# Kernel tuning notes

Hardware: AMD Instinct MI355X
Metric: run time of the kernel (lower is better)

## Reference

```python
import jax, jax.numpy as jnp
import numpy as np

NEG_INF = -1e30  # stands in for -inf; safe under fp16/bf16 softmax too


def setup_inputs() -> dict:
    key = jax.random.key(0)
    k1, k2, k3, k4 = jax.random.split(key, 4)
    B, M, N, V, A = 16, 512, 512, 1024, 1024
    q = jax.random.normal(k1, (B, M, V), dtype=jnp.float32)
    p = jax.random.normal(k2, (B, N, V), dtype=jnp.float32)
    q_mask = jnp.ones((B, M), dtype=jnp.int32)  # 1 = real token
    p_mask = jnp.ones((B, N), dtype=jnp.int32)
    # xavier_normal: std = sqrt(2/(fan_in+fan_out))
    std = np.sqrt(2.0 / (V + A)).astype(np.float32)
    W1 = jax.random.normal(k3, (A, V), dtype=jnp.float32) * std
    W2 = jax.random.normal(k4, (A, V), dtype=jnp.float32) * std
    return {"q": q, "p": p, "q_mask": q_mask, "p_mask": p_mask, "W1": W1, "W2": W2}


def reference(q, p, q_mask, p_mask, W1, W2):
    # Projections with ReLU (bias-free linears)
    s_q = jax.nn.relu(jnp.einsum('bmv,av->bma', q, W1))  # [B,M,A]
    s_p = jax.nn.relu(jnp.einsum('bnv,av->bna', p, W2))  # [B,N,A]
    # Shared score matrix s[b,m,n]
    s = jnp.einsum('bma,bna->bmn', s_q, s_p)
    # Direction 1: attend over p (mask pad columns of p), softmax over n
    s_to_p = jnp.where(p_mask[:, None, :] == 0, NEG_INF, s)
    weights_p = jax.nn.softmax(s_to_p, axis=2)            # [B,M,N]
    output_q = jnp.einsum('bmn,bnv->bmv', weights_p, p)   # [B,M,V]
    # Direction 2: transpose, attend over q (mask pad columns of q)
    s_to_q = jnp.where(q_mask[:, None, :] == 0, NEG_INF, jnp.swapaxes(s, 1, 2))
    weights_q = jax.nn.softmax(s_to_q, axis=2)            # [B,N,M]
    output_p = jnp.einsum('bnm,bmv->bnv', weights_q, q)   # [B,N,V]
    # Dropout is identity in eval mode (training=False)
    return (output_p, output_q)
```

## Files before the change

kernel.cpp:

```cpp
#include <hip/hip_runtime.h>


#define AS1 __attribute__((address_space(1)))
#define AS3 __attribute__((address_space(3)))

typedef _Float16 f16x8 __attribute__((ext_vector_type(8)));
typedef float f32x4 __attribute__((ext_vector_type(4)));

__device__ __forceinline__ long tswz(int r, int k, int ktiles) {
  return ((long)((r >> 7) * ktiles + (k >> 6 ? (k >> 5) : (k >> 5))) << 12)
       + ((long)(r & 127) << 5)
       + ((((k >> 3) & 3) ^ ((r >> 1) & 3)) << 3) + (k & 7);
}

__global__ __launch_bounds__(256) void prep_all(
    const float* __restrict__ q, const float* __restrict__ p,
    const float* __restrict__ W1, const float* __restrict__ W2,
    _Float16* __restrict__ xdst, _Float16* __restrict__ wdst)
{
  long g = (long)blockIdx.x * 256 + threadIdx.x;
  int rg = (int)(g >> 7);
  int c8 = ((int)g & 127) << 3;
  const float* srow;
  _Float16* dst;
  long off;
  if (rg < 8192) {
    srow = q + (long)rg * 1024 + c8; dst = xdst; off = tswz(rg, c8, 32);
  } else if (rg < 16384) {
    srow = p + (long)(rg - 8192) * 1024 + c8; dst = xdst; off = tswz(rg, c8, 32);
  } else {
    int r2 = rg - 16384;
    srow = (r2 < 1024 ? W1 + (long)r2 * 1024 : W2 + (long)(r2 - 1024) * 1024) + c8;
    dst = wdst; off = tswz(r2, c8, 32);
  }
  const float4* s4 = (const float4*)srow;
  float4 f0 = s4[0], f1 = s4[1];
  f16x8 hh;
  hh[0]=(_Float16)f0.x; hh[1]=(_Float16)f0.y; hh[2]=(_Float16)f0.z; hh[3]=(_Float16)f0.w;
  hh[4]=(_Float16)f1.x; hh[5]=(_Float16)f1.y; hh[6]=(_Float16)f1.z; hh[7]=(_Float16)f1.w;
  *(f16x8*)(dst + off) = hh;
}

__global__ __launch_bounds__(256) void prep_xT(
    const float* __restrict__ q, const float* __restrict__ p,
    _Float16* __restrict__ dstT)
{
  __shared__ float t[64][65];
  const int x = blockIdx.x, y = blockIdx.y, zz = blockIdx.z;
  const float* src = (zz < 16) ? (p + (long)zz * 524288)
                               : (q + (long)(zz - 16) * 524288);
  const int tid = threadIdx.x;
  for (int it = 0; it < 4; ++it) {
    int id = it * 256 + tid;
    int rr = id >> 4, cc = (id & 15) << 2;
    float4 f = *(const float4*)(src + (long)(y * 64 + rr) * 1024 + x * 64 + cc);
    t[rr][cc] = f.x; t[rr][cc + 1] = f.y; t[rr][cc + 2] = f.z; t[rr][cc + 3] = f.w;
  }
  __syncthreads();
  _Float16* db = dstT + (long)zz * 524288;
  for (int it = 0; it < 2; ++it) {
    int id = it * 256 + tid;
    int c = id >> 3, ch = id & 7;
    int v = x * 64 + c, mb = y * 64 + ch * 8;
    f16x8 hh;
#pragma unroll
    for (int i = 0; i < 8; ++i) hh[i] = (_Float16)t[ch * 8 + i][c];
    *(f16x8*)(db + tswz(v, mb, 16)) = hh;
  }
}

template<bool RELU, int OUTMODE>
__global__ __launch_bounds__(512, 2) void gemm256_dp(
    const _Float16* __restrict__ A, const _Float16* __restrict__ B,
    float* __restrict__ Cf, _Float16* __restrict__ Ch,
    const int ktiles, const int ldc,
    const long aBatchTiles, const long bBatchTiles, const long cBatchElems,
    const int cTilesRow, const long cOff0, const long cOff1, const int cSplit)
{
  __shared__ _Float16 sA[4][8192];
  __shared__ _Float16 sB[4][8192];

  const int gx = gridDim.x, gy = gridDim.y;
  long nwg = (long)gx * gy * gridDim.z;
  long bid = blockIdx.x + (long)gx * (blockIdx.y + (long)gy * blockIdx.z);
  long chunk = nwg >> 3;
  long o = (bid & 7) * chunk + (bid >> 3);
  const int bx = (int)(o % gx);
  const int by = (int)((o / gx) % gy);
  const int bz = (int)(o / ((long)gx * gy));

  const int tid = threadIdx.x;
  const int lane = tid & 63, w = tid >> 6;
  const int wm = w >> 2, wn = w & 3;
  const int lrow = lane & 15, kg = lane >> 4;
  const int swz = (lrow >> 1) & 3;

  const long aT0 = (long)bz * aBatchTiles + (long)(2 * by) * ktiles;
  const long bT0 = (long)bz * bBatchTiles + (long)(2 * bx) * ktiles;
  const int NKT = ktiles;

  auto stage = [&](int kt) {
    const int buf = kt & 3;
#pragma unroll
    for (int h = 0; h < 2; ++h) {
      __builtin_amdgcn_global_load_lds(
          (const AS1 void*)(A + ((aT0 + h * ktiles + kt) << 12) + w * 512 + lane * 8),
          (AS3 void*)(&sA[buf][h * 4096 + w * 512]), 16, 0, 0);
      __builtin_amdgcn_global_load_lds(
          (const AS1 void*)(B + ((bT0 + h * ktiles + kt) << 12) + w * 512 + lane * 8),
          (AS3 void*)(&sB[buf][h * 4096 + w * 512]), 16, 0, 0);
    }
  };

  const char* aF = (const char*)&sA[0][0] + wm * 8192 + lrow * 64 + ((kg ^ swz) << 4);
  const char* bF = (const char*)&sB[0][0] + (wn >> 1) * 8192
                 + ((wn & 1) * 64 + lrow) * 64 + ((kg ^ swz) << 4);

  f32x4 acc[8][4] = {};

  stage(0); stage(1); stage(2);

  for (int kt = 0; kt < NKT; ++kt) {
    if (kt < NKT - 2)       asm volatile("s_waitcnt vmcnt(8)" ::: "memory");
    else if (kt == NKT - 2) asm volatile("s_waitcnt vmcnt(4)" ::: "memory");
    else                    asm volatile("s_waitcnt vmcnt(0)" ::: "memory");
    __builtin_amdgcn_s_barrier();
    __builtin_amdgcn_sched_barrier(0);
    const int bo = (kt & 3) * 16384;
    f16x8 fa[8], fb[4];
#pragma unroll
    for (int i = 0; i < 8; ++i) fa[i] = *(const f16x8*)(aF + bo + i * 1024);
#pragma unroll
    for (int i = 0; i < 4; ++i) fb[i] = *(const f16x8*)(bF + bo + i * 1024);
    if (kt + 3 < NKT) stage(kt + 3);
    __builtin_amdgcn_s_setprio(1);
    if (OUTMODE == 1) {
#pragma unroll
      for (int aj = 0; aj < 8; ++aj)
#pragma unroll
        for (int bi = 0; bi < 4; ++bi)
          acc[aj][bi] = __builtin_amdgcn_mfma_f32_16x16x32_f16(fb[bi], fa[aj], acc[aj][bi], 0, 0, 0);
    } else {
#pragma unroll
      for (int mi = 0; mi < 8; ++mi)
#pragma unroll
        for (int ni = 0; ni < 4; ++ni)
          acc[mi][ni] = __builtin_amdgcn_mfma_f32_16x16x32_f16(fa[mi], fb[ni], acc[mi][ni], 0, 0, 0);
    }
    __builtin_amdgcn_s_setprio(0);
  }

  if (OUTMODE == 1) {
    long cbase = cSplit ? (bz < 16 ? cOff0 + (long)bz * cBatchElems
                                   : cOff1 + (long)(bz - 16) * cBatchElems)
                        : (long)bz * cBatchElems;
    float* Cb = Cf + cbase;
    const int m0 = by * 256 + wm * 128 + lrow;
    const int v0 = bx * 256 + wn * 64 + (kg << 2);
#pragma unroll
    for (int aj = 0; aj < 8; ++aj)
#pragma unroll
      for (int bi = 0; bi < 4; ++bi)
        *(f32x4*)(Cb + (long)(m0 + aj * 16) * ldc + v0 + bi * 16) = acc[aj][bi];
  } else {
    const int m0 = by * 256 + wm * 128 + (kg << 2);
    const int a0 = bx * 256 + wn * 64 + lrow;
#pragma unroll
    for (int mi = 0; mi < 8; ++mi)
#pragma unroll
      for (int ni = 0; ni < 4; ++ni)
#pragma unroll
        for (int r2 = 0; r2 < 4; ++r2) {
          int r = m0 + mi * 16 + r2, c = a0 + ni * 16;
          float x = acc[mi][ni][r2];
          if (RELU) x = fmaxf(x, 0.0f);
          Ch[(long)bz * cBatchElems + tswz(r, c, cTilesRow)] = (_Float16)x;
        }
  }
}

template<int NTERMS, bool RELU>
__global__ __launch_bounds__(256, 2) void gemm_dp(
    const _Float16* __restrict__ Ah, const _Float16* __restrict__ Al,
    const _Float16* __restrict__ B, float* __restrict__ Cf,
    const int ktiles, const int ldc,
    const long aBatchTiles, const long bBatchTiles, const long cBatchElems)
{
  __shared__ _Float16 sA[4][4096];
  __shared__ _Float16 sB[4][4096];

  const int gx = gridDim.x, gy = gridDim.y;
  long nwg = (long)gx * gy * gridDim.z;
  long bid = blockIdx.x + (long)gx * (blockIdx.y + (long)gy * blockIdx.z);
  long chunk = nwg >> 3;
  long o = (bid & 7) * chunk + (bid >> 3);
  const int bx = (int)(o % gx);
  const int by = (int)((o / gx) % gy);
  const int bz = (int)(o / ((long)gx * gy));

  const int tid = threadIdx.x;
  const int lane = tid & 63, w = tid >> 6;
  const int wa = w >> 1, wb = w & 1;
  const int lrow = lane & 15, kg = lane >> 4;
  const int swz = (lrow >> 1) & 3;

  const long aT0 = (long)bz * aBatchTiles + (long)by * ktiles;
  const long bT0 = (long)bz * bBatchTiles + (long)bx * ktiles;
  const int NKT = NTERMS * ktiles;

  auto stage = [&](int kt) {
    const int buf = kt & 3;
    int ktB = kt;
    const _Float16* As = Ah;
    if (NTERMS == 2 && kt >= ktiles) { As = Al; ktB = kt - ktiles; }
    const long ta = (aT0 + ktB) << 12;
    const long tb = (bT0 + ktB) << 12;
#pragma unroll
    for (int j = 0; j < 2; ++j) {
      __builtin_amdgcn_global_load_lds(
          (const AS1 void*)(As + ta + j * 2048 + w * 512 + lane * 8),
          (AS3 void*)(&sA[buf][j * 2048 + w * 512]), 16, 0, 0);
      __builtin_amdgcn_global_load_lds(
          (const AS1 void*)(B + tb + j * 2048 + w * 512 + lane * 8),
          (AS3 void*)(&sB[buf][j * 2048 + w * 512]), 16, 0, 0);
    }
  };

  const char* aF = (const char*)&sA[0][0] + (wa * 64 + lrow) * 64 + ((kg ^ swz) << 4);
  const char* bF = (const char*)&sB[0][0] + (wb * 64 + lrow) * 64 + ((kg ^ swz) << 4);

  f32x4 acc[4][4] = {};

  stage(0); stage(1); stage(2);

  for (int kt = 0; kt < NKT; ++kt) {
    if (kt < NKT - 2)       asm volatile("s_waitcnt vmcnt(8)" ::: "memory");
    else if (kt == NKT - 2) asm volatile("s_waitcnt vmcnt(4)" ::: "memory");
    else                    asm volatile("s_waitcnt vmcnt(0)" ::: "memory");
    __builtin_amdgcn_s_barrier();
    __builtin_amdgcn_sched_barrier(0);
    const int bo = (kt & 3) * 8192;
    f16x8 fa[4], fb[4];
#pragma unroll
    for (int i = 0; i < 4; ++i) fa[i] = *(const f16x8*)(aF + bo + i * 1024);
#pragma unroll
    for (int i = 0; i < 4; ++i) fb[i] = *(const f16x8*)(bF + bo + i * 1024);
    if (kt + 3 < NKT) stage(kt + 3);
    __builtin_amdgcn_s_setprio(1);
#pragma unroll
    for (int mi = 0; mi < 4; ++mi)
#pragma unroll
      for (int ni = 0; ni < 4; ++ni)
        acc[mi][ni] = __builtin_amdgcn_mfma_f32_16x16x32_f16(fa[mi], fb[ni], acc[mi][ni], 0, 0, 0);
    __builtin_amdgcn_s_setprio(0);
  }

  float* Cb = Cf + (long)bz * cBatchElems;
  const int r0 = by * 128 + wa * 64 + (kg << 2);
  const int c0 = bx * 128 + wb * 64 + lrow;
#pragma unroll
  for (int mi = 0; mi < 4; ++mi)
#pragma unroll
    for (int ni = 0; ni < 4; ++ni)
#pragma unroll
      for (int r2 = 0; r2 < 4; ++r2)
        Cb[(long)(r0 + mi * 16 + r2) * ldc + c0 + ni * 16] = acc[mi][ni][r2];
}

__global__ __launch_bounds__(256) void softmax_row(
    const float* __restrict__ S, const int* __restrict__ mask, _Float16* __restrict__ W)
{
  const int row = blockIdx.x, b = row >> 9, m = row & 511;
  const float* Sr = S + (long)row * 512;
  const int* mr = mask + (long)b * 512;
  const int tid = threadIdx.x;
  const int lane = tid & 63, wave = tid >> 6;
  __shared__ float red[4];

  float v0 = mr[tid] ? Sr[tid] : -1e30f;
  float v1 = mr[tid + 256] ? Sr[tid + 256] : -1e30f;
  float mx = fmaxf(v0, v1);
#pragma unroll
  for (int of = 32; of >= 1; of >>= 1) mx = fmaxf(mx, __shfl_xor(mx, of, 64));
  if (lane == 0) red[wave] = mx;
  __syncthreads();
  mx = fmaxf(fmaxf(red[0], red[1]), fmaxf(red[2], red[3]));
  __syncthreads();
  float e0 = __expf(v0 - mx), e1 = __expf(v1 - mx);
  float sm = e0 + e1;
#pragma unroll
  for (int of = 32; of >= 1; of >>= 1) sm += __shfl_xor(sm, of, 64);
  if (lane == 0) red[wave] = sm;
  __syncthreads();
  float inv = 1.0f / (red[0] + red[1] + red[2] + red[3]);

  _Float16* Wb = W + (long)b * 262144;
  Wb[tswz(m, tid, 16)] = (_Float16)(e0 * inv);
  Wb[tswz(m, tid + 256, 16)] = (_Float16)(e1 * inv);
}

__global__ __launch_bounds__(256) void softmax_col(
    const float* __restrict__ S, const int* __restrict__ mask, _Float16* __restrict__ W)
{
  __shared__ float ldsT[32][513];
  const int n0 = blockIdx.x * 32, b = blockIdx.y;
  const float* Sb = S + (long)b * 262144;
  const int* mr = mask + (long)b * 512;
  const int tid = threadIdx.x;
  const int lane = tid & 63, w = tid >> 6;

  for (int it = 0; it < 64; ++it) {
    int m = it * 8 + (tid >> 5);
    int c = tid & 31;
    float v = mr[m] ? Sb[(long)m * 512 + n0 + c] : -1e30f;
    ldsT[c][m] = v;
  }
  __syncthreads();

  _Float16* Wb = W + (long)b * 262144;
#pragma unroll
  for (int cc = 0; cc < 8; ++cc) {
    int col = w * 8 + cc;
    float v[8];
#pragma unroll
    for (int j = 0; j < 8; ++j) v[j] = ldsT[col][lane + 64 * j];
    float mx = v[0];
#pragma unroll
    for (int j = 1; j < 8; ++j) mx = fmaxf(mx, v[j]);
#pragma unroll
    for (int of = 32; of >= 1; of >>= 1) mx = fmaxf(mx, __shfl_xor(mx, of, 64));
    float e[8], sm = 0.0f;
#pragma unroll
    for (int j = 0; j < 8; ++j) { e[j] = __expf(v[j] - mx); sm += e[j]; }
#pragma unroll
    for (int of = 32; of >= 1; of >>= 1) sm += __shfl_xor(sm, of, 64);
    float inv = 1.0f / sm;
    int n = n0 + col;
#pragma unroll
    for (int j = 0; j < 8; ++j)
      Wb[tswz(n, lane + 64 * j, 16)] = (_Float16)(e[j] * inv);
  }
}

extern "C" void kernel_launch(void* const* d_in, const int* in_sizes, int n_in,
                              void* d_out, int out_size, void* d_ws, size_t ws_size,
                              hipStream_t stream) {
  const float* q = (const float*)d_in[0];
  const float* p = (const float*)d_in[1];
  const int* q_mask = (const int*)d_in[2];
  const int* p_mask = (const int*)d_in[3];
  const float* W1 = (const float*)d_in[4];
  const float* W2 = (const float*)d_in[5];
  float* out = (float*)d_out;

  char* ws = (char*)d_ws;
  const size_t MB = 1048576;
  _Float16* W1h = (_Float16*)(ws + 0 * MB);
  _Float16* qh  = (_Float16*)(ws + 4 * MB);
  _Float16* sqh = (_Float16*)(ws + 36 * MB);
  _Float16* sph = (_Float16*)(ws + 52 * MB);
  float*    s   = (float*)(ws + 4 * MB);
  _Float16* wp  = (_Float16*)(ws + 36 * MB);
  _Float16* pT  = (_Float16*)(ws + 52 * MB);

  dim3 blk(256);

  prep_all<<<9216, blk, 0, stream>>>(q, p, W1, W2, qh, W1h);

  gemm256_dp<true, 2><<<dim3(4, 32, 2), dim3(512), 0, stream>>>(
      qh, W1h, nullptr, sqh,
      32, 0,
      2048, 256, 8388608L,
      32, 0, 0, 0);

  gemm_dp<1, false><<<dim3(4, 4, 16), blk, 0, stream>>>(
      sqh, nullptr, sph, s, 32, 512,
      128, 128, 262144L);

  prep_xT<<<dim3(16, 8, 32), blk, 0, stream>>>(q, p, pT);

  softmax_row<<<8192, blk, 0, stream>>>(s, p_mask, wp);
  softmax_col<<<dim3(16, 16), blk, 0, stream>>>(s, q_mask, wp + 4194304);

  gemm256_dp<false, 1><<<dim3(4, 2, 32), dim3(512), 0, stream>>>(
      wp, pT, out, nullptr,
      16, 1024,
      64, 128, 524288L,
      0, 8388608L, 0L, 1);
}
```

Before: 154.7 us.

## Transpose from fp16 copies and vectorize GEMM epilogue stores

The transpose kernel now reads the already-converted fp16 tiled copy of q/p instead of the fp32 originals, which halves its read traffic, and it uses an fp16 shared tile. Both GEMM kernels swap MFMA operand order so each lane holds four consecutive columns. That lets the fp16 ReLU epilogue write f16x4 vectors and the fp32 score epilogue write f32x4 vectors instead of scalar stores. The workspace layout is reshuffled so the fp16 activations stay alive until the transpose runs, and a redundant expression in the swizzle helper is simplified.

```diff
diff --git a/kernel.cpp b/kernel.cpp
--- a/kernel.cpp
+++ b/kernel.cpp
@@ -5,10 +5,11 @@
 #define AS3 __attribute__((address_space(3)))
 
 typedef _Float16 f16x8 __attribute__((ext_vector_type(8)));
+typedef _Float16 f16x4 __attribute__((ext_vector_type(4)));
 typedef float f32x4 __attribute__((ext_vector_type(4)));
 
 __device__ __forceinline__ long tswz(int r, int k, int ktiles) {
-  return ((long)((r >> 7) * ktiles + (k >> 6 ? (k >> 5) : (k >> 5))) << 12)
+  return ((long)((r >> 7) * ktiles + (k >> 5)) << 12)
        + ((long)(r & 127) << 5)
        + ((((k >> 3) & 3) ^ ((r >> 1) & 3)) << 3) + (k & 7);
 }
@@ -41,20 +42,18 @@
   *(f16x8*)(dst + off) = hh;
 }
 
-__global__ __launch_bounds__(256) void prep_xT(
-    const float* __restrict__ q, const float* __restrict__ p,
-    _Float16* __restrict__ dstT)
-{
-  __shared__ float t[64][65];
+__global__ __launch_bounds__(256) void prep_xT2(
+    const _Float16* __restrict__ xh, _Float16* __restrict__ dstT)
+{
+  __shared__ _Float16 t[64][72];
   const int x = blockIdx.x, y = blockIdx.y, zz = blockIdx.z;
-  const float* src = (zz < 16) ? (p + (long)zz * 524288)
-                               : (q + (long)(zz - 16) * 524288);
-  const int tid = threadIdx.x;
-  for (int it = 0; it < 4; ++it) {
+  const int rbase = (zz < 16) ? (8192 + zz * 512) : ((zz - 16) * 512);
+  const int tid = threadIdx.x;
+  for (int it = 0; it < 2; ++it) {
     int id = it * 256 + tid;
-    int rr = id >> 4, cc = (id & 15) << 2;
-    float4 f = *(const float4*)(src + (long)(y * 64 + rr) * 1024 + x * 64 + cc);
-    t[rr][cc] = f.x; t[rr][cc + 1] = f.y; t[rr][cc + 2] = f.z; t[rr][cc + 3] = f.w;
+    int mloc = id >> 3, v8 = (id & 7) << 3;
+    f16x8 v = *(const f16x8*)(xh + tswz(rbase + y * 64 + mloc, x * 64 + v8, 32));
+    *(f16x8*)(&t[mloc][v8]) = v;
   }
   __syncthreads();
   _Float16* db = dstT + (long)zz * 524288;
@@ -64,7 +63,7 @@
     int v = x * 64 + c, mb = y * 64 + ch * 8;
     f16x8 hh;
 #pragma unroll
-    for (int i = 0; i < 8; ++i) hh[i] = (_Float16)t[ch * 8 + i][c];
+    for (int i = 0; i < 8; ++i) hh[i] = t[ch * 8 + i][c];
     *(f16x8*)(db + tswz(v, mb, 16)) = hh;
   }
 }
@@ -134,55 +133,47 @@
     for (int i = 0; i < 4; ++i) fb[i] = *(const f16x8*)(bF + bo + i * 1024);
     if (kt + 3 < NKT) stage(kt + 3);
     __builtin_amdgcn_s_setprio(1);
-    if (OUTMODE == 1) {
-#pragma unroll
-      for (int aj = 0; aj < 8; ++aj)
-#pragma unroll
-        for (int bi = 0; bi < 4; ++bi)
-          acc[aj][bi] = __builtin_amdgcn_mfma_f32_16x16x32_f16(fb[bi], fa[aj], acc[aj][bi], 0, 0, 0);
-    } else {
-#pragma unroll
-      for (int mi = 0; mi < 8; ++mi)
-#pragma unroll
-        for (int ni = 0; ni < 4; ++ni)
-          acc[mi][ni] = __builtin_amdgcn_mfma_f32_16x16x32_f16(fa[mi], fb[ni], acc[mi][ni], 0, 0, 0);
-    }
+#pragma unroll
+    for (int mi = 0; mi < 8; ++mi)
+#pragma unroll
+      for (int ni = 0; ni < 4; ++ni)
+        acc[mi][ni] = __builtin_amdgcn_mfma_f32_16x16x32_f16(fb[ni], fa[mi], acc[mi][ni], 0, 0, 0);
     __builtin_amdgcn_s_setprio(0);
   }
 
+  const int m0 = by * 256 + wm * 128 + lrow;
+  const int b0 = bx * 256 + wn * 64 + (kg << 2);
   if (OUTMODE == 1) {
     long cbase = cSplit ? (bz < 16 ? cOff0 + (long)bz * cBatchElems
                                    : cOff1 + (long)(bz - 16) * cBatchElems)
                         : (long)bz * cBatchElems;
     float* Cb = Cf + cbase;
-    const int m0 = by * 256 + wm * 128 + lrow;
-    const int v0 = bx * 256 + wn * 64 + (kg << 2);
-#pragma unroll
-    for (int aj = 0; aj < 8; ++aj)
-#pragma unroll
-      for (int bi = 0; bi < 4; ++bi)
-        *(f32x4*)(Cb + (long)(m0 + aj * 16) * ldc + v0 + bi * 16) = acc[aj][bi];
+#pragma unroll
+    for (int mi = 0; mi < 8; ++mi)
+#pragma unroll
+      for (int ni = 0; ni < 4; ++ni)
+        *(f32x4*)(Cb + (long)(m0 + mi * 16) * ldc + b0 + ni * 16) = acc[mi][ni];
   } else {
-    const int m0 = by * 256 + wm * 128 + (kg << 2);
-    const int a0 = bx * 256 + wn * 64 + lrow;
+    _Float16* Cb = Ch + (long)bz * cBatchElems;
 #pragma unroll
     for (int mi = 0; mi < 8; ++mi)
 #pragma unroll
-      for (int ni = 0; ni < 4; ++ni)
+      for (int ni = 0; ni < 4; ++ni) {
+        f16x4 hv;
 #pragma unroll
         for (int r2 = 0; r2 < 4; ++r2) {
-          int r = m0 + mi * 16 + r2, c = a0 + ni * 16;
           float x = acc[mi][ni][r2];
           if (RELU) x = fmaxf(x, 0.0f);
-          Ch[(long)bz * cBatchElems + tswz(r, c, cTilesRow)] = (_Float16)x;
+          hv[r2] = (_Float16)x;
         }
-  }
-}
-
-template<int NTERMS, bool RELU>
+        *(f16x4*)(Cb + tswz(m0 + mi * 16, b0 + ni * 16, cTilesRow)) = hv;
+      }
+  }
+}
+
 __global__ __launch_bounds__(256, 2) void gemm_dp(
-    const _Float16* __restrict__ Ah, const _Float16* __restrict__ Al,
-    const _Float16* __restrict__ B, float* __restrict__ Cf,
+    const _Float16* __restrict__ Ah, const _Float16* __restrict__ B,
+    float* __restrict__ Cf,
     const int ktiles, const int ldc,
     const long aBatchTiles, const long bBatchTiles, const long cBatchElems)
 {
@@ -206,19 +197,16 @@
 
   const long aT0 = (long)bz * aBatchTiles + (long)by * ktiles;
   const long bT0 = (long)bz * bBatchTiles + (long)bx * ktiles;
-  const int NKT = NTERMS * ktiles;
+  const int NKT = ktiles;
 
   auto stage = [&](int kt) {
     const int buf = kt & 3;
-    int ktB = kt;
-    const _Float16* As = Ah;
-    if (NTERMS == 2 && kt >= ktiles) { As = Al; ktB = kt - ktiles; }
-    const long ta = (aT0 + ktB) << 12;
-    const long tb = (bT0 + ktB) << 12;
+    const long ta = (aT0 + kt) << 12;
+    const long tb = (bT0 + kt) << 12;
 #pragma unroll
     for (int j = 0; j < 2; ++j) {
       __builtin_amdgcn_global_load_lds(
-          (const AS1 void*)(As + ta + j * 2048 + w * 512 + lane * 8),
+          (const AS1 void*)(Ah + ta + j * 2048 + w * 512 + lane * 8),
           (AS3 void*)(&sA[buf][j * 2048 + w * 512]), 16, 0, 0);
       __builtin_amdgcn_global_load_lds(
           (const AS1 void*)(B + tb + j * 2048 + w * 512 + lane * 8),
@@ -251,20 +239,18 @@
     for (int mi = 0; mi < 4; ++mi)
 #pragma unroll
       for (int ni = 0; ni < 4; ++ni)
-        acc[mi][ni] = __builtin_amdgcn_mfma_f32_16x16x32_f16(fa[mi], fb[ni], acc[mi][ni], 0, 0, 0);
+        acc[mi][ni] = __builtin_amdgcn_mfma_f32_16x16x32_f16(fb[ni], fa[mi], acc[mi][ni], 0, 0, 0);
     __builtin_amdgcn_s_setprio(0);
   }
 
   float* Cb = Cf + (long)bz * cBatchElems;
-  const int r0 = by * 128 + wa * 64 + (kg << 2);
-  const int c0 = bx * 128 + wb * 64 + lrow;
+  const int m0 = by * 128 + wa * 64 + lrow;
+  const int n0 = bx * 128 + wb * 64 + (kg << 2);
 #pragma unroll
   for (int mi = 0; mi < 4; ++mi)
 #pragma unroll
     for (int ni = 0; ni < 4; ++ni)
-#pragma unroll
-      for (int r2 = 0; r2 < 4; ++r2)
-        Cb[(long)(r0 + mi * 16 + r2) * ldc + c0 + ni * 16] = acc[mi][ni][r2];
+      *(f32x4*)(Cb + (long)(m0 + mi * 16) * ldc + n0 + ni * 16) = acc[mi][ni];
 }
 
 __global__ __launch_bounds__(256) void softmax_row(
@@ -358,10 +344,10 @@
   _Float16* W1h = (_Float16*)(ws + 0 * MB);
   _Float16* qh  = (_Float16*)(ws + 4 * MB);
   _Float16* sqh = (_Float16*)(ws + 36 * MB);
-  _Float16* sph = (_Float16*)(ws + 52 * MB);
-  float*    s   = (float*)(ws + 4 * MB);
-  _Float16* wp  = (_Float16*)(ws + 36 * MB);
-  _Float16* pT  = (_Float16*)(ws + 52 * MB);
+  float*    s   = (float*)(ws + 68 * MB);
+  _Float16* pT  = (_Float16*)(ws + 36 * MB);
+  _Float16* wp  = (_Float16*)(ws + 4 * MB);
+  _Float16* wq  = (_Float16*)(ws + 12 * MB);
 
   dim3 blk(256);
 
@@ -373,14 +359,14 @@
       2048, 256, 8388608L,
       32, 0, 0, 0);
 
-  gemm_dp<1, false><<<dim3(4, 4, 16), blk, 0, stream>>>(
-      sqh, nullptr, sph, s, 32, 512,
+  gemm_dp<<<dim3(4, 4, 16), blk, 0, stream>>>(
+      sqh, (_Float16*)(ws + 52 * MB), s, 32, 512,
       128, 128, 262144L);
 
-  prep_xT<<<dim3(16, 8, 32), blk, 0, stream>>>(q, p, pT);
+  prep_xT2<<<dim3(16, 8, 32), blk, 0, stream>>>(qh, pT);
 
   softmax_row<<<8192, blk, 0, stream>>>(s, p_mask, wp);
-  softmax_col<<<dim3(16, 16), blk, 0, stream>>>(s, q_mask, wp + 4194304);
+  softmax_col<<<dim3(16, 16), blk, 0, stream>>>(s, q_mask, wq);
 
   gemm256_dp<false, 1><<<dim3(4, 2, 32), dim3(512), 0, stream>>>(
       wp, pT, out, nullptr,
```

Result: faster. 151.5 us, median of 2 (-2.1%).
